# Performance work log

Hardware: AMD Instinct MI355X
Metric: run time of the kernel (lower is better)

## Reference

```python
import jax, jax.numpy as jnp
import numpy as np

B, N, MAX_V = 256, 16384, 64

def setup_inputs() -> dict:
    key = jax.random.key(0)
    ks = jax.random.split(key, 11)
    s = 0.02
    x = jax.random.normal(ks[0], (B, N, 5), dtype=jnp.float32)
    W1 = jax.random.normal(ks[1], (2, 32), dtype=jnp.float32) * s
    b1 = jnp.zeros((32,), jnp.float32)
    W2 = jax.random.normal(ks[2], (32, 64), dtype=jnp.float32) * s
    b2 = jnp.zeros((64,), jnp.float32)
    W3 = jax.random.normal(ks[3], (201, 256), dtype=jnp.float32) * s
    b3 = jnp.zeros((256,), jnp.float32)
    W4 = jax.random.normal(ks[4], (256, 128), dtype=jnp.float32) * s
    b4 = jnp.zeros((128,), jnp.float32)
    W5 = jax.random.normal(ks[5], (128, MAX_V * 4), dtype=jnp.float32) * s
    # existence-logit biases initialized to -2.0 (indices i*4+3)
    b5 = jnp.zeros((MAX_V * 4,), jnp.float32).at[jnp.arange(MAX_V) * 4 + 3].set(-2.0)
    return {"x": x, "W1": W1, "b1": b1, "W2": W2, "b2": b2,
            "W3": W3, "b3": b3, "W4": W4, "b4": b4, "W5": W5, "b5": b5}

def _pca_align(coords):
    # coords: [B,N,3]
    n = coords.shape[1]
    centroid = coords.mean(axis=1, keepdims=True)          # [B,1,3]
    centered = coords - centroid                           # [B,N,3]
    cov = jnp.einsum('bni,bnj->bij', centered, centered) / n
    evals, evecs = jnp.linalg.eigh(cov)                    # ascending
    evals = evals[:, ::-1]                                 # descending
    evecs = evecs[:, :, ::-1]
    # det sign fix on 3rd column
    det = jnp.linalg.det(evecs)
    evecs = evecs.at[:, :, 2].multiply(jnp.where(det < 0, -1.0, 1.0)[:, None])
    # deterministic sign: each axis points toward side with more mass (vectorized)
    proj = jnp.einsum('bnd,bde->bne', centered, evecs)     # [B,N,3]
    pos = (proj > 0).sum(axis=1)
    neg = (proj < 0).sum(axis=1)
    sign = jnp.where(neg > pos, -1.0, 1.0)                 # [B,3]
    evecs = evecs * sign[:, None, :]
    aligned = jnp.einsum('bnd,bde->bne', centered, evecs)  # [B,N,3]
    eig_norm = evals / (evals.sum(axis=1, keepdims=True) + 1e-8)
    extents = aligned.max(axis=1) - aligned.min(axis=1)    # [B,3]
    pca_features = jnp.concatenate([eig_norm, extents, centroid[:, 0]], axis=1)  # [B,9]
    return aligned, pca_features, evecs, centroid

def reference(x, W1, b1, W2, b2, W3, b3, W4, b4, W5, b5):
    coords = x[:, :, :3]
    sem = x[:, :, 3:]                                      # [B,N,2]
    aligned, pca_features, rot, centroid = _pca_align(coords)
    # per-point MLP
    pf = jax.nn.relu(sem @ W1 + b1)
    pf = jax.nn.relu(pf @ W2 + b2)                         # [B,N,64]
    gmax = pf.max(axis=1)
    gavg = pf.mean(axis=1)
    gstd = jnp.std(pf, axis=1, ddof=1)                     # torch.std is unbiased
    g = jnp.concatenate([gmax, gavg, gstd, pca_features], axis=1)  # [B,201]
    h = jax.nn.relu(g @ W3 + b3)
    h = jax.nn.relu(h @ W4 + b4)
    out = (h @ W5 + b5).reshape(x.shape[0], MAX_V, 4)      # [B,64,4]
    return out
```

## Files before the change

### kernel.cpp

```cpp
#include <hip/hip_runtime.h>
#include <math.h>

#define BATCH 256
#define NPTS  16384
#define TPB   256
#define MID_TPB 1024

#define P1_CHUNKS     8
#define P1_PTS_BLOCK  (NPTS / P1_CHUNKS)
#define P1_ITERS      8

#define PART_STRIDE 256

typedef __bf16 bf16x8  __attribute__((ext_vector_type(8)));
typedef float  floatx4 __attribute__((ext_vector_type(4)));
typedef float  floatx2 __attribute__((ext_vector_type(2)));

__global__ __launch_bounds__(TPB, 4)
void pass1_kernel(const float* __restrict__ x, const float* __restrict__ W1,
                  const float* __restrict__ b1, const float* __restrict__ W2,
                  const float* __restrict__ b2, float* __restrict__ ws) {
    const int b     = blockIdx.x;
    const int chunk = blockIdx.y;
    const int tid   = threadIdx.x;
    const int lane  = tid & 63;
    const int wave  = tid >> 6;
    const int quad  = lane >> 4;
    const int l15   = lane & 15;

    __shared__ floatx2 sem_lds[4][64];

    bf16x8  Bf[4];
    floatx4 biasC[4];
#pragma unroll
    for (int t = 0; t < 4; ++t) {
        int n = t * 16 + l15;
#pragma unroll
        for (int j = 0; j < 8; ++j)
            Bf[t][j] = (__bf16)W2[(quad * 8 + j) * 64 + n];
        float bb = b2[n];
        biasC[t] = (floatx4){bb, bb, bb, bb};
    }
    floatx2 w1a2[4], w1b2[4], b1r2[4];
#pragma unroll
    for (int jp = 0; jp < 4; ++jp) {
        int jj = quad * 8 + jp * 2;
        w1a2[jp] = (floatx2){W1[jj],      W1[jj + 1]};
        w1b2[jp] = (floatx2){W1[32 + jj], W1[32 + jj + 1]};
        b1r2[jp] = (floatx2){b1[jj],      b1[jj + 1]};
    }

    const floatx2 zero2 = {0.f, 0.f};
    float   vmaxr[4] = {0.f, 0.f, 0.f, 0.f};
    floatx2 vsum[4], vsq[4];
#pragma unroll
    for (int t = 0; t < 4; ++t) {
        vsum[t] = zero2;
        vsq[t]  = zero2;
    }
    float mo[9];
#pragma unroll
    for (int j = 0; j < 9; ++j) mo[j] = 0.f;

    const float* xb = x + ((size_t)b * NPTS + (size_t)chunk * P1_PTS_BLOCK) * 5;
    const float* pc = xb + (size_t)wave * (P1_ITERS * 64) * 5 + (size_t)lane * 5;

    float c0 = pc[0], c1 = pc[1], c2 = pc[2], s0 = pc[3], s1 = pc[4];

#pragma unroll 1
    for (int it = 0; it < P1_ITERS; ++it) {
        const float* pn = pc + ((it < P1_ITERS - 1) ? 320 : 0);
        float n0 = pn[0], n1 = pn[1], n2 = pn[2], n3 = pn[3], n4 = pn[4];

        sem_lds[wave][lane] = (floatx2){s0, s1};

        mo[0] += c0; mo[1] += c1; mo[2] += c2;
        mo[3] = fmaf(c0, c0, mo[3]); mo[4] = fmaf(c0, c1, mo[4]); mo[5] = fmaf(c0, c2, mo[5]);
        mo[6] = fmaf(c1, c1, mo[6]); mo[7] = fmaf(c1, c2, mo[7]); mo[8] = fmaf(c2, c2, mo[8]);

        floatx2 gsem[4];
#pragma unroll
        for (int g = 0; g < 4; ++g)
            gsem[g] = sem_lds[wave][g * 16 + l15];

#pragma unroll
        for (int g = 0; g < 4; ++g) {
            floatx2 G0 = {gsem[g][0], gsem[g][0]};
            floatx2 G1 = {gsem[g][1], gsem[g][1]};
            bf16x8 Af;
#pragma unroll
            for (int jp = 0; jp < 4; ++jp) {
                floatx2 h = __builtin_elementwise_fma(
                    G0, w1a2[jp], __builtin_elementwise_fma(G1, w1b2[jp], b1r2[jp]));
                h = __builtin_elementwise_max(h, zero2);
                Af[2 * jp]     = (__bf16)h[0];
                Af[2 * jp + 1] = (__bf16)h[1];
            }
#pragma unroll
            for (int t = 0; t < 4; ++t) {
                floatx4 D = __builtin_amdgcn_mfma_f32_16x16x32_bf16(Af, Bf[t], biasC[t], 0, 0, 0);
                vmaxr[t] = fmaxf(fmaxf(D[0], D[1]),
                                 fmaxf(fmaxf(D[2], D[3]), vmaxr[t]));
                floatx2 d01 = {D[0], D[1]}, d23 = {D[2], D[3]};
                floatx2 p01 = __builtin_elementwise_max(d01, zero2);
                floatx2 p23 = __builtin_elementwise_max(d23, zero2);
                vsum[t] += p01 + p23;
                vsq[t]   = __builtin_elementwise_fma(p01, p01,
                               __builtin_elementwise_fma(p23, p23, vsq[t]));
            }
        }

        c0 = n0; c1 = n1; c2 = n2; s0 = n3; s1 = n4;
        pc += 320;
    }

    float vmax[4], vs[4], vq[4];
#pragma unroll
    for (int t = 0; t < 4; ++t) {
        vmax[t] = vmaxr[t];
        vs[t]   = vsum[t][0] + vsum[t][1];
        vq[t]   = vsq[t][0] + vsq[t][1];
        vmax[t] = fmaxf(vmax[t], __shfl_xor(vmax[t], 16));
        vmax[t] = fmaxf(vmax[t], __shfl_xor(vmax[t], 32));
        vs[t] += __shfl_xor(vs[t], 16);
        vs[t] += __shfl_xor(vs[t], 32);
        vq[t] += __shfl_xor(vq[t], 16);
        vq[t] += __shfl_xor(vq[t], 32);
    }
#pragma unroll
    for (int j = 0; j < 9; ++j) {
        float v = mo[j];
#pragma unroll
        for (int o = 32; o > 0; o >>= 1) v += __shfl_xor(v, o);
        mo[j] = v;
    }

    __shared__ float red[4][201];
    if (quad == 0) {
#pragma unroll
        for (int t = 0; t < 4; ++t) {
            red[wave][t * 16 + l15]       = vmax[t];
            red[wave][64 + t * 16 + l15]  = vs[t];
            red[wave][128 + t * 16 + l15] = vq[t];
        }
    }
    if (lane == 0) {
#pragma unroll
        for (int j = 0; j < 9; ++j) red[wave][192 + j] = mo[j];
    }
    __syncthreads();

    if (tid < 201) {
        float v0 = red[0][tid], v1 = red[1][tid], v2 = red[2][tid], v3 = red[3][tid];
        float r = (tid < 64) ? fmaxf(fmaxf(v0, v1), fmaxf(v2, v3))
                             : (v0 + v1) + (v2 + v3);
        ws[(size_t)(b * P1_CHUNKS + chunk) * PART_STRIDE + tid] = r;
    }
}

__global__ __launch_bounds__(MID_TPB)
void mid_kernel(const float* __restrict__ x,
                const float* __restrict__ W3, const float* __restrict__ b3,
                const float* __restrict__ W4, const float* __restrict__ b4,
                const float* __restrict__ W5, const float* __restrict__ b5,
                const float* __restrict__ ws, float* __restrict__ out) {
    const int b = blockIdx.x, t = threadIdx.x;
    const int lane = t & 63, wave = t >> 6;

    __shared__ float comb[201];
    __shared__ float redmm[16][8];
    __shared__ float g[224];
    __shared__ float h1[256];
    __shared__ float h2[128];
    __shared__ float part[8][256];

    if (t < 201) {
        const float* base = ws + (size_t)b * P1_CHUNKS * PART_STRIDE + t;
        float acc = base[0];
        if (t < 64) {
#pragma unroll
            for (int i = 1; i < P1_CHUNKS; ++i) acc = fmaxf(acc, base[i * PART_STRIDE]);
        } else {
#pragma unroll
            for (int i = 1; i < P1_CHUNKS; ++i) acc += base[i * PART_STRIDE];
        }
        comb[t] = acc;
    }
    __syncthreads();

    const float nin = 1.0f / (float)NPTS;
    const float cx = comb[192] * nin, cy = comb[193] * nin, cz = comb[194] * nin;
    float A[3][3];
    A[0][0] = comb[195] * nin - cx * cx; A[0][1] = comb[196] * nin - cx * cy;
    A[0][2] = comb[197] * nin - cx * cz;
    A[1][1] = comb[198] * nin - cy * cy; A[1][2] = comb[199] * nin - cy * cz;
    A[2][2] = comb[200] * nin - cz * cz;
    A[1][0] = A[0][1]; A[2][0] = A[0][2]; A[2][1] = A[1][2];
    float V[3][3] = {{1, 0, 0}, {0, 1, 0}, {0, 0, 1}};
    {
        const int PP[3] = {0, 0, 1};
        const int QQ[3] = {1, 2, 2};
        for (int sweep = 0; sweep < 7; ++sweep) {
#pragma unroll
            for (int r3 = 0; r3 < 3; ++r3) {
                int p = PP[r3], q = QQ[r3];
                float apq = A[p][q];
                if (fabsf(apq) < 1e-35f) continue;
                float theta = (A[q][q] - A[p][p]) / (2.0f * apq);
                float tt = 1.0f / (fabsf(theta) + sqrtf(fmaf(theta, theta, 1.0f)));
                if (theta < 0.0f) tt = -tt;
                float c = 1.0f / sqrtf(fmaf(tt, tt, 1.0f)), s = tt * c;
                float apq_t = tt * apq;
                A[p][p] -= apq_t;
                A[q][q] += apq_t;
                A[p][q] = A[q][p] = 0.0f;
#pragma unroll
                for (int r = 0; r < 3; ++r) {
                    if (r != p && r != q) {
                        float arp = A[r][p], arq = A[r][q];
                        A[r][p] = A[p][r] = c * arp - s * arq;
                        A[r][q] = A[q][r] = s * arp + c * arq;
                    }
                    float vrp = V[r][p], vrq = V[r][q];
                    V[r][p] = c * vrp - s * vrq;
                    V[r][q] = s * vrp + c * vrq;
                }
            }
        }
    }
    float w0 = A[0][0], w1v = A[1][1], w2v = A[2][2];
    int i0 = 0, i1 = 1, i2 = 2, sw;
    {
        float wa = w0, wb = w1v, wc = w2v, swf;
        if (wa < wb) { sw = i0; i0 = i1; i1 = sw; swf = wa; wa = wb; wb = swf; }
        if (wa < wc) { sw = i0; i0 = i2; i2 = sw; swf = wa; wa = wc; wc = swf; }
        if (wb < wc) { sw = i1; i1 = i2; i2 = sw; swf = wb; wb = wc; wc = swf; }
    }
#define SEL3(a0, a1, a2, id) ((id) == 0 ? (a0) : ((id) == 1 ? (a1) : (a2)))
    const float e0x = SEL3(V[0][0], V[0][1], V[0][2], i0);
    const float e0y = SEL3(V[1][0], V[1][1], V[1][2], i0);
    const float e0z = SEL3(V[2][0], V[2][1], V[2][2], i0);
    const float e1x = SEL3(V[0][0], V[0][1], V[0][2], i1);
    const float e1y = SEL3(V[1][0], V[1][1], V[1][2], i1);
    const float e1z = SEL3(V[2][0], V[2][1], V[2][2], i1);
    const float e2x = SEL3(V[0][0], V[0][1], V[0][2], i2);
    const float e2y = SEL3(V[1][0], V[1][1], V[1][2], i2);
    const float e2z = SEL3(V[2][0], V[2][1], V[2][2], i2);
    const float esum = w0 + w1v + w2v + 1e-8f;
    const float ena = SEL3(w0, w1v, w2v, i0) / esum;
    const float enb = SEL3(w0, w1v, w2v, i1) / esum;
    const float enc = SEL3(w0, w1v, w2v, i2) / esum;
#undef SEL3

    const float* xb = x + (size_t)b * NPTS * 5;
    float mn[3] = {3.4e38f, 3.4e38f, 3.4e38f};
    float mx3[3] = {-3.4e38f, -3.4e38f, -3.4e38f};
#pragma unroll 8
    for (int i = 0; i < NPTS / MID_TPB; ++i) {
        const float* p = xb + (size_t)(i * MID_TPB + t) * 5;
        float c0 = p[0] - cx, c1 = p[1] - cy, c2 = p[2] - cz;
        float p0 = fmaf(c0, e0x, fmaf(c1, e0y, c2 * e0z));
        float p1 = fmaf(c0, e1x, fmaf(c1, e1y, c2 * e1z));
        float p2 = fmaf(c0, e2x, fmaf(c1, e2y, c2 * e2z));
        mn[0] = fminf(mn[0], p0); mx3[0] = fmaxf(mx3[0], p0);
        mn[1] = fminf(mn[1], p1); mx3[1] = fmaxf(mx3[1], p1);
        mn[2] = fminf(mn[2], p2); mx3[2] = fmaxf(mx3[2], p2);
    }
#pragma unroll
    for (int d = 0; d < 3; ++d) {
        float v = mx3[d];
#pragma unroll
        for (int o = 32; o > 0; o >>= 1) v = fmaxf(v, __shfl_xor(v, o));
        if (lane == 0) redmm[wave][d] = v;
        float u = mn[d];
#pragma unroll
        for (int o = 32; o > 0; o >>= 1) u = fminf(u, __shfl_xor(u, o));
        if (lane == 0) redmm[wave][4 + d] = u;
    }
    __syncthreads();

    if (t < 64) {
        g[t] = comb[t];
        float s = comb[64 + t], sq = comb[128 + t];
        float avg = s * (1.0f / NPTS);
        g[64 + t] = avg;
        float var = (sq - s * avg) / (float)(NPTS - 1);
        g[128 + t] = sqrtf(fmaxf(var, 0.f));
    } else if (t < 73) {
        int j = t - 64;
        if (j < 3) {
            g[192 + j] = (j == 0) ? ena : ((j == 1) ? enb : enc);
        } else if (j < 6) {
            int d = j - 3;
            float fmx = redmm[0][d], fmn = redmm[0][4 + d];
#pragma unroll
            for (int w2 = 1; w2 < 16; ++w2) {
                fmx = fmaxf(fmx, redmm[w2][d]);
                fmn = fminf(fmn, redmm[w2][4 + d]);
            }
            g[195 + d] = fmx - fmn;
        } else {
            int d = j - 6;
            g[198 + d] = (d == 0) ? cx : ((d == 1) ? cy : cz);
        }
    }
    __syncthreads();

    {
        int p = t >> 8, c = t & 255;
        int j0 = p * 51, j1 = min(201, j0 + 51);
        float a = 0.f;
        for (int j = j0; j < j1; ++j) a = fmaf(g[j], W3[j * 256 + c], a);
        part[p][c] = a;
    }
    __syncthreads();
    if (t < 256) {
        float a = b3[t] + (part[0][t] + part[1][t]) + (part[2][t] + part[3][t]);
        h1[t] = fmaxf(a, 0.f);
    }
    __syncthreads();
    {
        int p = t >> 7, c = t & 127;
        int j0 = p * 32;
        float a = 0.f;
#pragma unroll
        for (int j = j0; j < j0 + 32; ++j) a = fmaf(h1[j], W4[j * 128 + c], a);
        part[p][c] = a;
    }
    __syncthreads();
    if (t < 128) {
        float a = b4[t];
#pragma unroll
        for (int p = 0; p < 8; ++p) a += part[p][t];
        h2[t] = fmaxf(a, 0.f);
    }
    __syncthreads();
    {
        int p = t >> 8, c = t & 255;
        int j0 = p * 32;
        float a = 0.f;
#pragma unroll
        for (int j = j0; j < j0 + 32; ++j) a = fmaf(h2[j], W5[j * 256 + c], a);
        part[p][c] = a;
    }
    __syncthreads();
    if (t < 256) {
        float o = b5[t] + (part[0][t] + part[1][t]) + (part[2][t] + part[3][t]);
        out[(size_t)b * 256 + t] = o;
    }
}

extern "C" void kernel_launch(void* const* d_in, const int* in_sizes, int n_in,
                              void* d_out, int out_size, void* d_ws, size_t ws_size,
                              hipStream_t stream) {
    const float* x  = (const float*)d_in[0];
    const float* W1 = (const float*)d_in[1];
    const float* b1 = (const float*)d_in[2];
    const float* W2 = (const float*)d_in[3];
    const float* b2 = (const float*)d_in[4];
    const float* W3 = (const float*)d_in[5];
    const float* b3 = (const float*)d_in[6];
    const float* W4 = (const float*)d_in[7];
    const float* b4 = (const float*)d_in[8];
    const float* W5 = (const float*)d_in[9];
    const float* b5 = (const float*)d_in[10];
    float* out = (float*)d_out;
    float* ws  = (float*)d_ws;

    pass1_kernel<<<dim3(BATCH, P1_CHUNKS), TPB, 0, stream>>>(x, W1, b1, W2, b2, ws);
    mid_kernel<<<dim3(BATCH), MID_TPB, 0, stream>>>(x, W3, b3, W4, b4, W5, b5, ws, out);
}
```

Baseline: 204.2 us.

## Split extent pass into separate chunked kernel to spread second x read

The min/max pass over PCA-aligned coordinates moves out of the per-batch mid kernel (256 blocks of 1024 threads) into a new ext_kernel launched over batch×8 chunks. Each chunk block recomputes the 3x3 eigendecomposition redundantly and writes partial extents to the workspace, which the final MLP kernel then reduces. The aim is to spread the second full read of x across more blocks and CUs. The cost is an extra kernel launch and repeated eigh work in every chunk block.

```diff
diff --git a/kernel.cpp b/kernel.cpp
--- a/kernel.cpp
+++ b/kernel.cpp
@@ -15,6 +15,75 @@
 typedef __bf16 bf16x8  __attribute__((ext_vector_type(8)));
 typedef float  floatx4 __attribute__((ext_vector_type(4)));
 typedef float  floatx2 __attribute__((ext_vector_type(2)));
+
+__device__ __forceinline__ void eigh3(const float mo9[9],
+    float& cx, float& cy, float& cz,
+    float& e0x, float& e0y, float& e0z,
+    float& e1x, float& e1y, float& e1z,
+    float& e2x, float& e2y, float& e2z,
+    float& ena, float& enb, float& enc) {
+    const float nin = 1.0f / (float)NPTS;
+    cx = mo9[0] * nin; cy = mo9[1] * nin; cz = mo9[2] * nin;
+    float A[3][3];
+    A[0][0] = mo9[3] * nin - cx * cx; A[0][1] = mo9[4] * nin - cx * cy;
+    A[0][2] = mo9[5] * nin - cx * cz;
+    A[1][1] = mo9[6] * nin - cy * cy; A[1][2] = mo9[7] * nin - cy * cz;
+    A[2][2] = mo9[8] * nin - cz * cz;
+    A[1][0] = A[0][1]; A[2][0] = A[0][2]; A[2][1] = A[1][2];
+    float V[3][3] = {{1, 0, 0}, {0, 1, 0}, {0, 0, 1}};
+    const int PP[3] = {0, 0, 1};
+    const int QQ[3] = {1, 2, 2};
+    for (int sweep = 0; sweep < 7; ++sweep) {
+#pragma unroll
+        for (int r3 = 0; r3 < 3; ++r3) {
+            int p = PP[r3], q = QQ[r3];
+            float apq = A[p][q];
+            if (fabsf(apq) < 1e-35f) continue;
+            float theta = (A[q][q] - A[p][p]) / (2.0f * apq);
+            float tt = 1.0f / (fabsf(theta) + sqrtf(fmaf(theta, theta, 1.0f)));
+            if (theta < 0.0f) tt = -tt;
+            float c = 1.0f / sqrtf(fmaf(tt, tt, 1.0f)), s = tt * c;
+            float apq_t = tt * apq;
+            A[p][p] -= apq_t;
+            A[q][q] += apq_t;
+            A[p][q] = A[q][p] = 0.0f;
+#pragma unroll
+            for (int r = 0; r < 3; ++r) {
+                if (r != p && r != q) {
+                    float arp = A[r][p], arq = A[r][q];
+                    A[r][p] = A[p][r] = c * arp - s * arq;
+                    A[r][q] = A[q][r] = s * arp + c * arq;
+                }
+                float vrp = V[r][p], vrq = V[r][q];
+                V[r][p] = c * vrp - s * vrq;
+                V[r][q] = s * vrp + c * vrq;
+            }
+        }
+    }
+    float w0 = A[0][0], w1v = A[1][1], w2v = A[2][2];
+    int i0 = 0, i1 = 1, i2 = 2, sw;
+    {
+        float wa = w0, wb = w1v, wc = w2v, swf;
+        if (wa < wb) { sw = i0; i0 = i1; i1 = sw; swf = wa; wa = wb; wb = swf; }
+        if (wa < wc) { sw = i0; i0 = i2; i2 = sw; swf = wa; wa = wc; wc = swf; }
+        if (wb < wc) { sw = i1; i1 = i2; i2 = sw; swf = wb; wb = wc; wc = swf; }
+    }
+#define SEL3(a0, a1, a2, id) ((id) == 0 ? (a0) : ((id) == 1 ? (a1) : (a2)))
+    e0x = SEL3(V[0][0], V[0][1], V[0][2], i0);
+    e0y = SEL3(V[1][0], V[1][1], V[1][2], i0);
+    e0z = SEL3(V[2][0], V[2][1], V[2][2], i0);
+    e1x = SEL3(V[0][0], V[0][1], V[0][2], i1);
+    e1y = SEL3(V[1][0], V[1][1], V[1][2], i1);
+    e1z = SEL3(V[2][0], V[2][1], V[2][2], i1);
+    e2x = SEL3(V[0][0], V[0][1], V[0][2], i2);
+    e2y = SEL3(V[1][0], V[1][1], V[1][2], i2);
+    e2z = SEL3(V[2][0], V[2][1], V[2][2], i2);
+    const float esum = w0 + w1v + w2v + 1e-8f;
+    ena = SEL3(w0, w1v, w2v, i0) / esum;
+    enb = SEL3(w0, w1v, w2v, i1) / esum;
+    enc = SEL3(w0, w1v, w2v, i2) / esum;
+#undef SEL3
+}
 
 __global__ __launch_bounds__(TPB, 4)
 void pass1_kernel(const float* __restrict__ x, const float* __restrict__ W1,
@@ -158,17 +227,67 @@
     }
 }
 
+__global__ __launch_bounds__(TPB)
+void ext_kernel(const float* __restrict__ x, const float* __restrict__ ws_in,
+                float* __restrict__ ws) {
+    const int b = blockIdx.x, chunk = blockIdx.y, t = threadIdx.x;
+    const int lane = t & 63, wv = t >> 6;
+
+    const float* wrow = ws_in + (size_t)b * P1_CHUNKS * PART_STRIDE;
+    float m9[9];
+#pragma unroll
+    for (int j = 0; j < 9; ++j) {
+        float a = 0.f;
+#pragma unroll
+        for (int i = 0; i < P1_CHUNKS; ++i) a += wrow[i * PART_STRIDE + 192 + j];
+        m9[j] = a;
+    }
+    float cx, cy, cz, e0x, e0y, e0z, e1x, e1y, e1z, e2x, e2y, e2z, ena, enb, enc;
+    eigh3(m9, cx, cy, cz, e0x, e0y, e0z, e1x, e1y, e1z, e2x, e2y, e2z, ena, enb, enc);
+
+    const float* xb = x + ((size_t)b * NPTS + (size_t)chunk * P1_PTS_BLOCK) * 5;
+    float mn0 = 3.4e38f, mn1 = 3.4e38f, mn2 = 3.4e38f;
+    float mx0 = -3.4e38f, mx1 = -3.4e38f, mx2 = -3.4e38f;
+#pragma unroll
+    for (int i = 0; i < P1_PTS_BLOCK / TPB; ++i) {
+        const float* p = xb + (size_t)(i * TPB + t) * 5;
+        float c0 = p[0] - cx, c1 = p[1] - cy, c2 = p[2] - cz;
+        float p0 = fmaf(c0, e0x, fmaf(c1, e0y, c2 * e0z));
+        float p1 = fmaf(c0, e1x, fmaf(c1, e1y, c2 * e1z));
+        float p2 = fmaf(c0, e2x, fmaf(c1, e2y, c2 * e2z));
+        mn0 = fminf(mn0, p0); mx0 = fmaxf(mx0, p0);
+        mn1 = fminf(mn1, p1); mx1 = fmaxf(mx1, p1);
+        mn2 = fminf(mn2, p2); mx2 = fmaxf(mx2, p2);
+    }
+    __shared__ float red2[4][6];
+#pragma unroll
+    for (int o = 32; o > 0; o >>= 1) {
+        mn0 = fminf(mn0, __shfl_xor(mn0, o)); mx0 = fmaxf(mx0, __shfl_xor(mx0, o));
+        mn1 = fminf(mn1, __shfl_xor(mn1, o)); mx1 = fmaxf(mx1, __shfl_xor(mx1, o));
+        mn2 = fminf(mn2, __shfl_xor(mn2, o)); mx2 = fmaxf(mx2, __shfl_xor(mx2, o));
+    }
+    if (lane == 0) {
+        red2[wv][0] = mn0; red2[wv][1] = mn1; red2[wv][2] = mn2;
+        red2[wv][3] = mx0; red2[wv][4] = mx1; red2[wv][5] = mx2;
+    }
+    __syncthreads();
+    if (t < 6) {
+        float a = red2[0][t];
+#pragma unroll
+        for (int w = 1; w < 4; ++w)
+            a = (t < 3) ? fminf(a, red2[w][t]) : fmaxf(a, red2[w][t]);
+        ws[(size_t)(b * P1_CHUNKS + chunk) * PART_STRIDE + 208 + t] = a;
+    }
+}
+
 __global__ __launch_bounds__(MID_TPB)
-void mid_kernel(const float* __restrict__ x,
-                const float* __restrict__ W3, const float* __restrict__ b3,
-                const float* __restrict__ W4, const float* __restrict__ b4,
-                const float* __restrict__ W5, const float* __restrict__ b5,
-                const float* __restrict__ ws, float* __restrict__ out) {
+void final_kernel(const float* __restrict__ W3, const float* __restrict__ b3,
+                  const float* __restrict__ W4, const float* __restrict__ b4,
+                  const float* __restrict__ W5, const float* __restrict__ b5,
+                  const float* __restrict__ ws, float* __restrict__ out) {
     const int b = blockIdx.x, t = threadIdx.x;
-    const int lane = t & 63, wave = t >> 6;
 
     __shared__ float comb[201];
-    __shared__ float redmm[16][8];
     __shared__ float g[224];
     __shared__ float h1[256];
     __shared__ float h2[128];
@@ -188,96 +307,11 @@
     }
     __syncthreads();
 
-    const float nin = 1.0f / (float)NPTS;
-    const float cx = comb[192] * nin, cy = comb[193] * nin, cz = comb[194] * nin;
-    float A[3][3];
-    A[0][0] = comb[195] * nin - cx * cx; A[0][1] = comb[196] * nin - cx * cy;
-    A[0][2] = comb[197] * nin - cx * cz;
-    A[1][1] = comb[198] * nin - cy * cy; A[1][2] = comb[199] * nin - cy * cz;
-    A[2][2] = comb[200] * nin - cz * cz;
-    A[1][0] = A[0][1]; A[2][0] = A[0][2]; A[2][1] = A[1][2];
-    float V[3][3] = {{1, 0, 0}, {0, 1, 0}, {0, 0, 1}};
-    {
-        const int PP[3] = {0, 0, 1};
-        const int QQ[3] = {1, 2, 2};
-        for (int sweep = 0; sweep < 7; ++sweep) {
-#pragma unroll
-            for (int r3 = 0; r3 < 3; ++r3) {
-                int p = PP[r3], q = QQ[r3];
-                float apq = A[p][q];
-                if (fabsf(apq) < 1e-35f) continue;
-                float theta = (A[q][q] - A[p][p]) / (2.0f * apq);
-                float tt = 1.0f / (fabsf(theta) + sqrtf(fmaf(theta, theta, 1.0f)));
-                if (theta < 0.0f) tt = -tt;
-                float c = 1.0f / sqrtf(fmaf(tt, tt, 1.0f)), s = tt * c;
-                float apq_t = tt * apq;
-                A[p][p] -= apq_t;
-                A[q][q] += apq_t;
-                A[p][q] = A[q][p] = 0.0f;
-#pragma unroll
-                for (int r = 0; r < 3; ++r) {
-                    if (r != p && r != q) {
-                        float arp = A[r][p], arq = A[r][q];
-                        A[r][p] = A[p][r] = c * arp - s * arq;
-                        A[r][q] = A[q][r] = s * arp + c * arq;
-                    }
-                    float vrp = V[r][p], vrq = V[r][q];
-                    V[r][p] = c * vrp - s * vrq;
-                    V[r][q] = s * vrp + c * vrq;
-                }
-            }
-        }
-    }
-    float w0 = A[0][0], w1v = A[1][1], w2v = A[2][2];
-    int i0 = 0, i1 = 1, i2 = 2, sw;
-    {
-        float wa = w0, wb = w1v, wc = w2v, swf;
-        if (wa < wb) { sw = i0; i0 = i1; i1 = sw; swf = wa; wa = wb; wb = swf; }
-        if (wa < wc) { sw = i0; i0 = i2; i2 = sw; swf = wa; wa = wc; wc = swf; }
-        if (wb < wc) { sw = i1; i1 = i2; i2 = sw; swf = wb; wb = wc; wc = swf; }
-    }
-#define SEL3(a0, a1, a2, id) ((id) == 0 ? (a0) : ((id) == 1 ? (a1) : (a2)))
-    const float e0x = SEL3(V[0][0], V[0][1], V[0][2], i0);
-    const float e0y = SEL3(V[1][0], V[1][1], V[1][2], i0);
-    const float e0z = SEL3(V[2][0], V[2][1], V[2][2], i0);
-    const float e1x = SEL3(V[0][0], V[0][1], V[0][2], i1);
-    const float e1y = SEL3(V[1][0], V[1][1], V[1][2], i1);
-    const float e1z = SEL3(V[2][0], V[2][1], V[2][2], i1);
-    const float e2x = SEL3(V[0][0], V[0][1], V[0][2], i2);
-    const float e2y = SEL3(V[1][0], V[1][1], V[1][2], i2);
-    const float e2z = SEL3(V[2][0], V[2][1], V[2][2], i2);
-    const float esum = w0 + w1v + w2v + 1e-8f;
-    const float ena = SEL3(w0, w1v, w2v, i0) / esum;
-    const float enb = SEL3(w0, w1v, w2v, i1) / esum;
-    const float enc = SEL3(w0, w1v, w2v, i2) / esum;
-#undef SEL3
-
-    const float* xb = x + (size_t)b * NPTS * 5;
-    float mn[3] = {3.4e38f, 3.4e38f, 3.4e38f};
-    float mx3[3] = {-3.4e38f, -3.4e38f, -3.4e38f};
-#pragma unroll 8
-    for (int i = 0; i < NPTS / MID_TPB; ++i) {
-        const float* p = xb + (size_t)(i * MID_TPB + t) * 5;
-        float c0 = p[0] - cx, c1 = p[1] - cy, c2 = p[2] - cz;
-        float p0 = fmaf(c0, e0x, fmaf(c1, e0y, c2 * e0z));
-        float p1 = fmaf(c0, e1x, fmaf(c1, e1y, c2 * e1z));
-        float p2 = fmaf(c0, e2x, fmaf(c1, e2y, c2 * e2z));
-        mn[0] = fminf(mn[0], p0); mx3[0] = fmaxf(mx3[0], p0);
-        mn[1] = fminf(mn[1], p1); mx3[1] = fmaxf(mx3[1], p1);
-        mn[2] = fminf(mn[2], p2); mx3[2] = fmaxf(mx3[2], p2);
-    }
-#pragma unroll
-    for (int d = 0; d < 3; ++d) {
-        float v = mx3[d];
-#pragma unroll
-        for (int o = 32; o > 0; o >>= 1) v = fmaxf(v, __shfl_xor(v, o));
-        if (lane == 0) redmm[wave][d] = v;
-        float u = mn[d];
-#pragma unroll
-        for (int o = 32; o > 0; o >>= 1) u = fminf(u, __shfl_xor(u, o));
-        if (lane == 0) redmm[wave][4 + d] = u;
-    }
-    __syncthreads();
+    float m9[9];
+#pragma unroll
+    for (int j = 0; j < 9; ++j) m9[j] = comb[192 + j];
+    float cx, cy, cz, e0x, e0y, e0z, e1x, e1y, e1z, e2x, e2y, e2z, ena, enb, enc;
+    eigh3(m9, cx, cy, cz, e0x, e0y, e0z, e1x, e1y, e1z, e2x, e2y, e2z, ena, enb, enc);
 
     if (t < 64) {
         g[t] = comb[t];
@@ -292,13 +326,14 @@
             g[192 + j] = (j == 0) ? ena : ((j == 1) ? enb : enc);
         } else if (j < 6) {
             int d = j - 3;
-            float fmx = redmm[0][d], fmn = redmm[0][4 + d];
-#pragma unroll
-            for (int w2 = 1; w2 < 16; ++w2) {
-                fmx = fmaxf(fmx, redmm[w2][d]);
-                fmn = fminf(fmn, redmm[w2][4 + d]);
+            const float* wrow = ws + (size_t)b * P1_CHUNKS * PART_STRIDE;
+            float mn = wrow[208 + d], mx = wrow[211 + d];
+#pragma unroll
+            for (int i = 1; i < P1_CHUNKS; ++i) {
+                mn = fminf(mn, wrow[i * PART_STRIDE + 208 + d]);
+                mx = fmaxf(mx, wrow[i * PART_STRIDE + 211 + d]);
             }
-            g[195 + d] = fmx - fmn;
+            g[195 + d] = mx - mn;
         } else {
             int d = j - 6;
             g[198 + d] = (d == 0) ? cx : ((d == 1) ? cy : cz);
@@ -368,5 +403,6 @@
     float* ws  = (float*)d_ws;
 
     pass1_kernel<<<dim3(BATCH, P1_CHUNKS), TPB, 0, stream>>>(x, W1, b1, W2, b2, ws);
-    mid_kernel<<<dim3(BATCH), MID_TPB, 0, stream>>>(x, W3, b3, W4, b4, W5, b5, ws, out);
+    ext_kernel<<<dim3(BATCH, P1_CHUNKS), TPB, 0, stream>>>(x, ws, ws);
+    final_kernel<<<dim3(BATCH), MID_TPB, 0, stream>>>(W3, b3, W4, b4, W5, b5, ws, out);
 }
```

New measurement: 218.0 us. 1.07x slower.
